# Kernel tuning notes

Measured on AMD Instinct MI355X. Metric: run time of the kernel, lower is better.

Reference implementation:

```python
import jax, jax.numpy as jnp
import numpy as np

B, S, D = 2, 2048, 2048
H, KV, HD = 32, 8, 64
REP = H // KV  # query heads per kv head
SCALE = np.float32(1.0 / np.sqrt(HD))


def setup_inputs() -> dict:
    key = jax.random.key(0)
    ks = jax.random.split(key, 5)
    x = jax.random.normal(ks[0], (B, S, D), dtype=jnp.float32)
    # RoPE tables: standard rotate_half convention, cos/sin shape [S, HD]
    inv_freq = 1.0 / (10000.0 ** (jnp.arange(0, HD, 2, dtype=jnp.float32) / HD))
    freqs = jnp.outer(jnp.arange(S, dtype=jnp.float32), inv_freq)  # [S, HD/2]
    emb = jnp.concatenate([freqs, freqs], axis=-1)  # [S, HD]
    cos, sin = jnp.cos(emb), jnp.sin(emb)
    std = np.float32(0.02)
    Wq = jax.random.normal(ks[1], (D, H * HD), dtype=jnp.float32) * std
    Wk = jax.random.normal(ks[2], (D, KV * HD), dtype=jnp.float32) * std
    Wv = jax.random.normal(ks[3], (D, KV * HD), dtype=jnp.float32) * std
    Wo = jax.random.normal(ks[4], (H * HD, D), dtype=jnp.float32) * std
    return {"x": x, "cos": cos, "sin": sin, "Wq": Wq, "Wk": Wk, "Wv": Wv, "Wo": Wo}


def _rotate_half(u):
    u1, u2 = jnp.split(u, 2, axis=-1)
    return jnp.concatenate([-u2, u1], axis=-1)


def reference(x, cos, sin, Wq, Wk, Wv, Wo):
    # projections -> [B, heads, S, HD]
    q = (x @ Wq).reshape(B, S, H, HD).transpose(0, 2, 1, 3)
    k = (x @ Wk).reshape(B, S, KV, HD).transpose(0, 2, 1, 3)
    v = (x @ Wv).reshape(B, S, KV, HD).transpose(0, 2, 1, 3)
    # RoPE on q and k (cos/sin broadcast over batch & head dims)
    c, s = cos[None, None], sin[None, None]
    q = q * c + _rotate_half(q) * s
    k = k * c + _rotate_half(k) * s
    # GQA: group query heads per kv head instead of materializing repeat_kv
    qg = q.reshape(B, KV, REP, S, HD)
    scores = jnp.einsum('bgrqd,bgkd->bgrqk', qg, k) * SCALE  # [B,KV,REP,S,S]
    causal = jnp.tril(jnp.ones((S, S), dtype=bool))
    scores = jnp.where(causal, scores, jnp.float32(-1e30))
    attn = jax.nn.softmax(scores, axis=-1)
    out = jnp.einsum('bgrqk,bgkd->bgrqd', attn, v)  # [B,KV,REP,S,HD]
    out = out.reshape(B, H, S, HD).transpose(0, 2, 1, 3).reshape(B, S, H * HD)
    return out @ Wo
```

## Files before the change

### kernel.cpp

```cpp
#include <hip/hip_runtime.h>

typedef unsigned short u16;
typedef __bf16 bfx8 __attribute__((ext_vector_type(8)));
typedef float f32x4 __attribute__((ext_vector_type(4)));
typedef float f32x16 __attribute__((ext_vector_type(16)));

#define MFMA16(a,b,c) __builtin_amdgcn_mfma_f32_16x16x32_bf16(a,b,c,0,0,0)
#define MFMA32(a,b,c) __builtin_amdgcn_mfma_f32_32x32x16_bf16(a,b,c,0,0,0)

__device__ __forceinline__ u16 f2bf(float f) {
  union { float f; unsigned u; } v; v.f = f;
  unsigned r = v.u + 0x7fffu + ((v.u >> 16) & 1u);
  return (u16)(r >> 16);
}

__device__ __forceinline__ unsigned cvtpk(float lo, float hi) {
  unsigned r;
  asm("v_cvt_pk_bf16_f32 %0, %1, %2" : "=v"(r) : "v"(lo), "v"(hi));
  return r;
}

__device__ __forceinline__ void swap32(unsigned &a, unsigned &b) {
  asm("v_permlane32_swap_b32 %0, %1" : "+v"(a), "+v"(b));
}

__device__ __forceinline__ void gld16(const void* g, void* l) {
  __builtin_amdgcn_global_load_lds(
      (const __attribute__((address_space(1))) unsigned int*)g,
      (__attribute__((address_space(3))) unsigned int*)l, 16, 0, 0);
}


__global__ void afrag_k(const float* __restrict__ in, u16* __restrict__ Af) {
  int i = blockIdx.x * 256 + threadIdx.x;
  int sm = i >> 8, d0 = (i & 255) * 8;
  const float* p = in + (size_t)sm * 2048 + d0;
  float4 a = *(const float4*)p;
  float4 b = *(const float4*)(p + 4);
  union { u16 h[8]; uint4 u; } o;
  o.h[0]=f2bf(a.x); o.h[1]=f2bf(a.y); o.h[2]=f2bf(a.z); o.h[3]=f2bf(a.w);
  o.h[4]=f2bf(b.x); o.h[5]=f2bf(b.y); o.h[6]=f2bf(b.z); o.h[7]=f2bf(b.w);
  int mt = sm >> 4, kt = d0 >> 5, lp = (sm & 15) + ((d0 >> 3) & 3) * 16;
  *(uint4*)(Af + ((size_t)(mt * 64 + kt) * 512 + lp * 8)) = o.u;
}

__global__ void bfrag_k(const float* __restrict__ W, u16* __restrict__ Bf,
                        int N, int ntoff) {
  __shared__ float tile[32][72];
  int nb = blockIdx.x, kb = blockIdx.y;
  int t = threadIdx.x;
  int r = t >> 3, c8 = (t & 7) * 8;
  const float* src = W + (size_t)(kb * 32 + r) * N + nb * 64 + c8;
  *(float4*)&tile[r][c8]     = *(const float4*)src;
  *(float4*)&tile[r][c8 + 4] = *(const float4*)(src + 4);
  __syncthreads();
  int fb = t >> 6, l = t & 63;
  int nn = fb * 16 + (l & 15), k0 = (l >> 4) * 8;
  union { u16 h[8]; uint4 u; } o;
  #pragma unroll
  for (int j = 0; j < 8; j++) o.h[j] = f2bf(tile[k0 + j][nn]);
  *(uint4*)(Bf + ((size_t)((ntoff + nb * 4 + fb) * 64 + kb) * 512 + l * 8)) = o.u;
}

__global__ __launch_bounds__(256, 3) void gemm_qkv(
    const u16* __restrict__ Af, const u16* __restrict__ Bf,
    const float* __restrict__ cosT, const float* __restrict__ sinT,
    u16* __restrict__ Qf, u16* __restrict__ Kf, u16* __restrict__ Vf) {
  __shared__ u16 lds[2 * 20 * 512];
  const int tid = threadIdx.x, lane = tid & 63, w = tid >> 6;
  const int lrow = lane & 15, lg = lane >> 4;
  const int nwg = gridDim.x;
  const int per = nwg >> 3;
  const int swz = ((int)blockIdx.x & 7) * per + ((int)blockIdx.x >> 3);
  const int bm = swz / 12, bn = swz % 12;
  const int bm4 = bm * 4, bn16 = bn * 16;
  const int KT = 64;

  f32x4 acc[4][4] = {};
  u16* buf0 = lds;
  u16* buf1 = lds + 20 * 512;

  auto stageB = [&](int s, u16* dst) {
    #pragma unroll
    for (int j = 0; j < 4; j++) {
      int ng = w * 4 + j;
      gld16(Bf + ((size_t)(bn16 + ng) * KT + s) * 512 + lane * 8,
            dst + (4 + ng) * 512);
    }
  };
  auto stageA = [&](int s, u16* dst) {
    gld16(Af + ((size_t)(bm4 + w) * KT + s) * 512 + lane * 8,
          dst + w * 512);
  };

  stageB(0, buf0); stageA(0, buf0);
  stageB(1, buf1); stageA(1, buf1);
  asm volatile("s_waitcnt vmcnt(5)" ::: "memory");
  __builtin_amdgcn_s_barrier();

  bfx8 ar[2], br[4];
  for (int t = 0; t < KT; t++) {
    u16* rb = (t & 1) ? buf1 : buf0;
    const int s2 = (t + 2 < KT) ? t + 2 : 0;
    #pragma unroll
    for (int i = 0; i < 2; i++)
      ar[i] = *(const bfx8*)(rb + i * 512 + lane * 8);
    #pragma unroll
    for (int j = 0; j < 4; j++)
      br[j] = *(const bfx8*)(rb + (4 + w * 4 + j) * 512 + lane * 8);
    asm volatile("s_waitcnt lgkmcnt(0)" ::: "memory");
    __builtin_amdgcn_s_barrier();
    stageB(s2, rb);
    __builtin_amdgcn_s_setprio(1);
    #pragma unroll
    for (int i = 0; i < 2; i++)
      #pragma unroll
      for (int j = 0; j < 4; j++)
        acc[i][j] = MFMA16(ar[i], br[j], acc[i][j]);
    __builtin_amdgcn_s_setprio(0);
    __builtin_amdgcn_s_barrier();
    #pragma unroll
    for (int i = 0; i < 2; i++)
      ar[i] = *(const bfx8*)(rb + (2 + i) * 512 + lane * 8);
    asm volatile("s_waitcnt lgkmcnt(0)" ::: "memory");
    __builtin_amdgcn_s_barrier();
    stageA(s2, rb);
    __builtin_amdgcn_s_setprio(1);
    #pragma unroll
    for (int i = 0; i < 2; i++)
      #pragma unroll
      for (int j = 0; j < 4; j++)
        acc[2 + i][j] = MFMA16(ar[i], br[j], acc[2 + i][j]);
    __builtin_amdgcn_s_setprio(0);
    asm volatile("s_waitcnt vmcnt(5)" ::: "memory");
    __builtin_amdgcn_s_barrier();
  }
  asm volatile("s_waitcnt vmcnt(0)" ::: "memory");
  __builtin_amdgcn_s_barrier();

  const int hh = bn * 4 + w;
  const int m0 = bm * 64;
  u16* otw = lds + w * 2048;
  char* otb = (char*)otw;

  #pragma unroll
  for (int half = 0; half < 2; half++) {
    const int rowbase = m0 + half * 32;
    const int bb = rowbase >> 11;
    const int s0 = rowbase & 2047;
    if (hh < 40) {
      const float qsc = (hh < 32) ? 0.18033688f : 1.0f;
      #pragma unroll
      for (int mgl = 0; mgl < 2; mgl++) {
        const int mg = half * 2 + mgl;
        #pragma unroll
        for (int ng = 0; ng < 2; ng++) {
          const int d1 = ng * 16 + lrow;
          #pragma unroll
          for (int r = 0; r < 4; r++) {
            int s = s0 + mgl * 16 + lg * 4 + r;
            float a  = acc[mg][ng][r];
            float a2 = acc[mg][ng + 2][r];
            float c1 = cosT[s * 64 + d1],      s1v = sinT[s * 64 + d1];
            float c2 = cosT[s * 64 + d1 + 32], s2v = sinT[s * 64 + d1 + 32];
            float o1 = (a * c1 - a2 * s1v) * qsc;
            float o2 = (a2 * c2 + a * s2v) * qsc;
            int srow = mgl * 16 + lg * 4 + r;
            int swzb = (srow & 7) << 4;
            *(u16*)(otb + ((srow * 128 + d1 * 2) ^ swzb)) = f2bf(o1);
            *(u16*)(otb + ((srow * 128 + (d1 + 32) * 2) ^ swzb)) = f2bf(o2);
          }
        }
      }
      const int qt = s0 >> 5;
      u16* dst = (hh < 32)
          ? Qf + ((size_t)(bb * 32 + hh) * 64 + qt) * 2048
          : Kf + ((size_t)(bb * 8 + (hh - 32)) * 64 + qt) * 2048;
      const int srw = lane & 31;
      const int d0 = (lane >> 5) * 8;
      #pragma unroll
      for (int ks = 0; ks < 4; ks++) {
        int byte = ((srw * 128 + (ks * 16 + d0) * 2)) ^ ((srw & 7) << 4);
        uint4 v = *(uint4*)(otb + byte);
        *(uint4*)(dst + ks * 512 + lane * 8) = v;
      }
    } else {
      #pragma unroll
      for (int mgl = 0; mgl < 2; mgl++) {
        const int mg = half * 2 + mgl;
        #pragma unroll
        for (int ng = 0; ng < 4; ng++) {
          const int d = ng * 16 + lrow;
          #pragma unroll
          for (int r = 0; r < 4; r++) {
            int srow = mgl * 16 + lg * 4 + r;
            *(u16*)(otb + ((srow * 128 + d * 2) ^ ((srow & 7) << 4))) =
                f2bf(acc[mg][ng][r]);
          }
        }
      }
      const int kt = s0 >> 6;
      const int g = hh - 40;
      u16* dst = Vf + ((size_t)(bb * 8 + g) * 32 + kt) * 4096;
      const int d = lane & 31;
      const int hi8 = (lane >> 5) * 8;
      #pragma unroll
      for (int ks2 = 0; ks2 < 2; ks2++) {
        const int ks = half * 2 + ks2;
        #pragma unroll
        for (int sub = 0; sub < 2; sub++) {
          const int dd = sub * 32 + d;
          union { u16 h[8]; uint4 u; } o;
          #pragma unroll
          for (int j = 0; j < 8; j++) {
            int srow = ks2 * 16 + hi8 + j;
            o.h[j] = *(u16*)(otb + ((srow * 128 + dd * 2) ^ ((srow & 7) << 4)));
          }
          *(uint4*)(dst + (sub * 4 + ks) * 512 + lane * 8) = o.u;
        }
      }
    }
    __builtin_amdgcn_s_barrier();
  }
}

__global__ __launch_bounds__(256, 3) void gemm8p(
    const u16* __restrict__ Af, const u16* __restrict__ Bf,
    float* __restrict__ C, int N, int KT, int nbx) {
  __shared__ u16 lds[2 * 20 * 512];
  const int tid = threadIdx.x, lane = tid & 63, w = tid >> 6;
  const int lrow = lane & 15, lg = lane >> 4;
  const int nwg = gridDim.x;
  const int per = nwg >> 3;
  const int swz = ((int)blockIdx.x & 7) * per + ((int)blockIdx.x >> 3);
  const int bm = swz / nbx, bn = swz % nbx;
  const int bm4 = bm * 4, bn16 = bn * 16;
  const int T = KT;

  f32x4 acc[4][4] = {};
  u16* buf0 = lds;
  u16* buf1 = lds + 20 * 512;

  auto stageB = [&](int s, u16* dst) {
    #pragma unroll
    for (int j = 0; j < 4; j++) {
      int ng = w * 4 + j;
      gld16(Bf + ((size_t)(bn16 + ng) * KT + s) * 512 + lane * 8,
            dst + (4 + ng) * 512);
    }
  };
  auto stageA = [&](int s, u16* dst) {
    gld16(Af + ((size_t)(bm4 + w) * KT + s) * 512 + lane * 8,
          dst + w * 512);
  };

  stageB(0, buf0); stageA(0, buf0);
  stageB(1, buf1); stageA(1, buf1);
  asm volatile("s_waitcnt vmcnt(5)" ::: "memory");
  __builtin_amdgcn_s_barrier();

  bfx8 ar[2], br[4];
  for (int t = 0; t < T; t++) {
    u16* rb = (t & 1) ? buf1 : buf0;
    const int s2 = (t + 2 < T) ? t + 2 : 0;
    #pragma unroll
    for (int i = 0; i < 2; i++)
      ar[i] = *(const bfx8*)(rb + i * 512 + lane * 8);
    #pragma unroll
    for (int j = 0; j < 4; j++)
      br[j] = *(const bfx8*)(rb + (4 + w * 4 + j) * 512 + lane * 8);
    asm volatile("s_waitcnt lgkmcnt(0)" ::: "memory");
    __builtin_amdgcn_s_barrier();
    stageB(s2, rb);
    __builtin_amdgcn_s_setprio(1);
    #pragma unroll
    for (int i = 0; i < 2; i++)
      #pragma unroll
      for (int j = 0; j < 4; j++)
        acc[i][j] = MFMA16(ar[i], br[j], acc[i][j]);
    __builtin_amdgcn_s_setprio(0);
    __builtin_amdgcn_s_barrier();
    #pragma unroll
    for (int i = 0; i < 2; i++)
      ar[i] = *(const bfx8*)(rb + (2 + i) * 512 + lane * 8);
    asm volatile("s_waitcnt lgkmcnt(0)" ::: "memory");
    __builtin_amdgcn_s_barrier();
    stageA(s2, rb);
    __builtin_amdgcn_s_setprio(1);
    #pragma unroll
    for (int i = 0; i < 2; i++)
      #pragma unroll
      for (int j = 0; j < 4; j++)
        acc[2 + i][j] = MFMA16(ar[i], br[j], acc[2 + i][j]);
    __builtin_amdgcn_s_setprio(0);
    asm volatile("s_waitcnt vmcnt(5)" ::: "memory");
    __builtin_amdgcn_s_barrier();
  }
  asm volatile("s_waitcnt vmcnt(0)" ::: "memory");

  const int m0 = bm * 64, n0 = bn * 256 + w * 64;
  #pragma unroll
  for (int mg = 0; mg < 4; mg++) {
    int row = m0 + mg * 16 + lg * 4;
    #pragma unroll
    for (int ng = 0; ng < 4; ng++) {
      int col = n0 + ng * 16 + lrow;
      float* cp = C + (size_t)row * N + col;
      #pragma unroll
      for (int r = 0; r < 4; r++) cp[(size_t)r * N] = acc[mg][ng][r];
    }
  }
}

__global__ __launch_bounds__(256, 2) void attn_k(
    const u16* __restrict__ Qf, const u16* __restrict__ Kf,
    const u16* __restrict__ Vf, u16* __restrict__ Aof)
{
  __shared__ u16 ot[4][32 * 64];
  const int tid = threadIdx.x, lane = tid & 63, w = tid >> 6;
  const int h = blockIdx.y, b = blockIdx.z;
  const int kvh = h >> 2;
  const int ql = lane & 31, hi = lane >> 5;
  const int qrA = blockIdx.x * 4 + w;

  const u16* Qh = Qf + (size_t)(b * 32 + h) * 131072;
  const u16* Kp = Kf + (size_t)(b * 8 + kvh) * 131072 + lane * 8;
  const u16* Vp = Vf + (size_t)(b * 8 + kvh) * 131072 + lane * 8;

  #pragma unroll
  for (int half = 0; half < 2; half++) {
    const int qr = half ? qrA : 63 - qrA;
    const int q0 = qr * 32;
    const int qg = q0 + ql;
    const int nkt = qr / 2 + 1;

    bfx8 qf[4];
    #pragma unroll
    for (int ks = 0; ks < 4; ks++)
      qf[ks] = *(const bfx8*)(Qh + (size_t)qr * 2048 + ks * 512 + lane * 8);

    f32x16 oacc0 = {}, oacc1 = {};
    float lsv[8] = {};

    const u16* Kt = Kp;
    const u16* Vt = Vp;
    bfx8 ka[8];
    #pragma unroll
    for (int i = 0; i < 8; i++)
      ka[i] = *(const bfx8*)(Kt + i * 512);

    #pragma unroll 2
    for (int kt = 0; kt < nkt; kt++) {
      const int kb = kt * 64;
      bfx8 va[8];
      #pragma unroll
      for (int i = 0; i < 8; i++)
        va[i] = *(const bfx8*)(Vt + i * 512);
      f32x16 st0 = {}, st1 = {};
      #pragma unroll
      for (int ks = 0; ks < 4; ks++) {
        st0 = MFMA32(ka[ks], qf[ks], st0);
        st1 = MFMA32(ka[4 + ks], qf[ks], st1);
      }
      const u16* Kn = (kt + 1 < nkt) ? Kt + 4096 : Kp;
      bfx8 kn[8];
      #pragma unroll
      for (int i = 0; i < 8; i++)
        kn[i] = *(const bfx8*)(Kn + i * 512);
      if (kt == nkt - 1) {
        #pragma unroll
        for (int r = 0; r < 16; r++) {
          int crow = (r & 3) + 8 * (r >> 2) + 4 * hi;
          if (kb + crow > qg) st0[r] = -3.0e38f;
          if (kb + 32 + crow > qg) st1[r] = -3.0e38f;
        }
      }
      #pragma unroll
      for (int r = 0; r < 16; r++) { st0[r] = exp2f(st0[r]); }
      #pragma unroll
      for (int r = 0; r < 16; r++) { st1[r] = exp2f(st1[r]); }
      #pragma unroll
      for (int r = 0; r < 16; r++) lsv[r & 7] += st0[r] + st1[r];
      bfx8 pb[4];
      #pragma unroll
      for (int ks = 0; ks < 4; ks++) {
        int o = (ks & 1) * 8;
        unsigned X = cvtpk(ks < 2 ? st0[o + 0] : st1[o + 0], ks < 2 ? st0[o + 1] : st1[o + 1]);
        unsigned Z = cvtpk(ks < 2 ? st0[o + 2] : st1[o + 2], ks < 2 ? st0[o + 3] : st1[o + 3]);
        unsigned Y = cvtpk(ks < 2 ? st0[o + 4] : st1[o + 4], ks < 2 ? st0[o + 5] : st1[o + 5]);
        unsigned W = cvtpk(ks < 2 ? st0[o + 6] : st1[o + 6], ks < 2 ? st0[o + 7] : st1[o + 7]);
        swap32(X, Y);
        swap32(Z, W);
        union { unsigned u[4]; bfx8 v; } uu;
        uu.u[0] = X; uu.u[1] = Z; uu.u[2] = Y; uu.u[3] = W;
        pb[ks] = uu.v;
      }
      #pragma unroll
      for (int ks = 0; ks < 4; ks++) {
        oacc0 = MFMA32(va[ks], pb[ks], oacc0);
        oacc1 = MFMA32(va[4 + ks], pb[ks], oacc1);
      }
      #pragma unroll
      for (int i = 0; i < 8; i++) ka[i] = kn[i];
      Kt += 4096;
      Vt += 4096;
    }
    float lsum = ((lsv[0] + lsv[1]) + (lsv[2] + lsv[3])) +
                 ((lsv[4] + lsv[5]) + (lsv[6] + lsv[7]));
    lsum += __shfl_xor(lsum, 32);
    float inv = 1.f / lsum;
    u16* my = ot[w];
    #pragma unroll
    for (int dt = 0; dt < 2; dt++) {
      #pragma unroll
      for (int g = 0; g < 4; g++) {
        float a0 = (dt ? oacc1[g*4+0] : oacc0[g*4+0]) * inv;
        float a1 = (dt ? oacc1[g*4+1] : oacc0[g*4+1]) * inv;
        float a2 = (dt ? oacc1[g*4+2] : oacc0[g*4+2]) * inv;
        float a3 = (dt ? oacc1[g*4+3] : oacc0[g*4+3]) * inv;
        unsigned w0 = cvtpk(a0, a1), w1 = cvtpk(a2, a3);
        int d = dt * 32 + g * 8 + 4 * hi;
        int byte = (ql * 128 + d * 2) ^ ((ql & 7) << 4);
        *(uint2*)((char*)my + byte) = make_uint2(w0, w1);
      }
    }
    #pragma unroll
    for (int rr = 0; rr < 4; rr++) {
      int q = rr * 8 + (lane >> 3);
      int dk = (lane & 7) * 8;
      int byte = (q * 128 + dk * 2) ^ ((q & 7) << 4);
      uint4 val = *(uint4*)((char*)my + byte);
      int mt = b * 128 + qr * 2 + (q >> 4);
      int ktg = h * 2 + (dk >> 5);
      int lp = (q & 15) + ((dk >> 3) & 3) * 16;
      *(uint4*)(Aof + ((size_t)(mt * 64 + ktg) * 512 + lp * 8)) = val;
    }
  }
}

extern "C" void kernel_launch(void* const* d_in, const int* in_sizes, int n_in,
                              void* d_out, int out_size, void* d_ws, size_t ws_size,
                              hipStream_t stream) {
  const float* x    = (const float*)d_in[0];
  const float* cosT = (const float*)d_in[1];
  const float* sinT = (const float*)d_in[2];
  const float* Wq   = (const float*)d_in[3];
  const float* Wk   = (const float*)d_in[4];
  const float* Wv   = (const float*)d_in[5];
  const float* Wo   = (const float*)d_in[6];
  float* out = (float*)d_out;
  char* ws = (char*)d_ws;

  u16* Af   = (u16*)(ws);
  u16* Bqkv = (u16*)(ws + 16777216);
  u16* Bwo  = (u16*)(ws + 29360128);
  u16* Qf   = (u16*)(ws + 37748736);
  u16* Kf   = (u16*)(ws + 54525952);
  u16* Vf   = (u16*)(ws + 58720256);
  u16* Aof  = (u16*)(ws + 62914560);

  afrag_k<<<4096, 256, 0, stream>>>(x, Af);
  bfrag_k<<<dim3(32, 64), 256, 0, stream>>>(Wq, Bqkv, 2048, 0);
  bfrag_k<<<dim3(8, 64), 256, 0, stream>>>(Wk, Bqkv, 512, 128);
  bfrag_k<<<dim3(8, 64), 256, 0, stream>>>(Wv, Bqkv, 512, 160);
  bfrag_k<<<dim3(32, 64), 256, 0, stream>>>(Wo, Bwo, 2048, 0);

  gemm_qkv<<<768, 256, 0, stream>>>(Af, Bqkv, cosT, sinT, Qf, Kf, Vf);

  attn_k<<<dim3(8, 32, 2), 256, 0, stream>>>(Qf, Kf, Vf, Aof);

  gemm8p<<<512, 256, 0, stream>>>(Aof, Bwo, out, 2048, 64, 8);
}
```

Measured before the change: 186.8 us.

## Enlarge QKV GEMM tile to 256x256 with 8 waves and 4-stage LDS ring

The fused QKV projection GEMM moves from 256-thread blocks with 64-row M tiles to 512-thread blocks that each cover 256 rows, with 8 waves laid out 2x4. Global loads go into a four-slot LDS ring prefetched three K-steps ahead instead of double buffering. The aim is more operand reuse per LDS load, less global traffic and deeper latency hiding. In exchange there is more LDS (128KB) and more accumulator registers, and only 192 workgroups, which may leave CUs poorly occupied. The epilogue is adapted to write four 32-row chunks per wave, and the per-chunk barrier is dropped.

```diff
diff --git a/kernel.cpp b/kernel.cpp
--- a/kernel.cpp
+++ b/kernel.cpp
@@ -62,97 +62,97 @@
   *(uint4*)(Bf + ((size_t)((ntoff + nb * 4 + fb) * 64 + kb) * 512 + l * 8)) = o.u;
 }
 
-__global__ __launch_bounds__(256, 3) void gemm_qkv(
+__global__ __launch_bounds__(512, 2) void gemm_qkv(
     const u16* __restrict__ Af, const u16* __restrict__ Bf,
     const float* __restrict__ cosT, const float* __restrict__ sinT,
     u16* __restrict__ Qf, u16* __restrict__ Kf, u16* __restrict__ Vf) {
-  __shared__ u16 lds[2 * 20 * 512];
+  __shared__ u16 lds[65536];
   const int tid = threadIdx.x, lane = tid & 63, w = tid >> 6;
+  const int wm = w >> 2, wn = w & 3;
   const int lrow = lane & 15, lg = lane >> 4;
   const int nwg = gridDim.x;
   const int per = nwg >> 3;
   const int swz = ((int)blockIdx.x & 7) * per + ((int)blockIdx.x >> 3);
   const int bm = swz / 12, bn = swz % 12;
-  const int bm4 = bm * 4, bn16 = bn * 16;
-  const int KT = 64;
-
-  f32x4 acc[4][4] = {};
-  u16* buf0 = lds;
-  u16* buf1 = lds + 20 * 512;
-
-  auto stageB = [&](int s, u16* dst) {
-    #pragma unroll
-    for (int j = 0; j < 4; j++) {
-      int ng = w * 4 + j;
-      gld16(Bf + ((size_t)(bn16 + ng) * KT + s) * 512 + lane * 8,
-            dst + (4 + ng) * 512);
+  const int bm16 = bm * 16, bn16 = bn * 16;
+  const int NG = 64;
+
+  f32x4 acc[8][4] = {};
+
+  auto stage2 = [&](int g, int ph) {
+    int gs = (g < NG) ? g : 0;
+    u16* sl = lds + (g & 3) * 16384;
+    #pragma unroll
+    for (int j = 0; j < 2; j++) {
+      int bi = w * 4 + ph * 2 + j;
+      const u16* src = (bi < 16)
+        ? Af + ((size_t)(bm16 + bi) * NG + gs) * 512 + lane * 8
+        : Bf + ((size_t)(bn16 + (bi - 16)) * NG + gs) * 512 + lane * 8;
+      gld16(src, sl + bi * 512);
     }
   };
-  auto stageA = [&](int s, u16* dst) {
-    gld16(Af + ((size_t)(bm4 + w) * KT + s) * 512 + lane * 8,
-          dst + w * 512);
-  };
-
-  stageB(0, buf0); stageA(0, buf0);
-  stageB(1, buf1); stageA(1, buf1);
-  asm volatile("s_waitcnt vmcnt(5)" ::: "memory");
+
+  stage2(0, 0); stage2(0, 1);
+  stage2(1, 0); stage2(1, 1);
+  stage2(2, 0); stage2(2, 1);
+  asm volatile("s_waitcnt vmcnt(8)" ::: "memory");
   __builtin_amdgcn_s_barrier();
 
-  bfx8 ar[2], br[4];
-  for (int t = 0; t < KT; t++) {
-    u16* rb = (t & 1) ? buf1 : buf0;
-    const int s2 = (t + 2 < KT) ? t + 2 : 0;
-    #pragma unroll
-    for (int i = 0; i < 2; i++)
-      ar[i] = *(const bfx8*)(rb + i * 512 + lane * 8);
+  bfx8 ar[4], br[4];
+  for (int g = 0; g < NG; g++) {
+    u16* sl = lds + (g & 3) * 16384;
     #pragma unroll
     for (int j = 0; j < 4; j++)
-      br[j] = *(const bfx8*)(rb + (4 + w * 4 + j) * 512 + lane * 8);
+      br[j] = *(const bfx8*)(sl + (16 + wn * 4 + j) * 512 + lane * 8);
+    #pragma unroll
+    for (int i = 0; i < 4; i++)
+      ar[i] = *(const bfx8*)(sl + (wm * 8 + i) * 512 + lane * 8);
+    stage2(g + 3, 0);
+    __builtin_amdgcn_s_barrier();
     asm volatile("s_waitcnt lgkmcnt(0)" ::: "memory");
-    __builtin_amdgcn_s_barrier();
-    stageB(s2, rb);
+    __builtin_amdgcn_sched_barrier(0);
     __builtin_amdgcn_s_setprio(1);
     #pragma unroll
-    for (int i = 0; i < 2; i++)
+    for (int i = 0; i < 4; i++)
       #pragma unroll
       for (int j = 0; j < 4; j++)
         acc[i][j] = MFMA16(ar[i], br[j], acc[i][j]);
     __builtin_amdgcn_s_setprio(0);
     __builtin_amdgcn_s_barrier();
     #pragma unroll
-    for (int i = 0; i < 2; i++)
-      ar[i] = *(const bfx8*)(rb + (2 + i) * 512 + lane * 8);
+    for (int i = 0; i < 4; i++)
+      ar[i] = *(const bfx8*)(sl + (wm * 8 + 4 + i) * 512 + lane * 8);
+    stage2(g + 3, 1);
+    __builtin_amdgcn_s_barrier();
     asm volatile("s_waitcnt lgkmcnt(0)" ::: "memory");
-    __builtin_amdgcn_s_barrier();
-    stageA(s2, rb);
+    __builtin_amdgcn_sched_barrier(0);
     __builtin_amdgcn_s_setprio(1);
     #pragma unroll
-    for (int i = 0; i < 2; i++)
+    for (int i = 0; i < 4; i++)
       #pragma unroll
       for (int j = 0; j < 4; j++)
-        acc[2 + i][j] = MFMA16(ar[i], br[j], acc[2 + i][j]);
+        acc[4 + i][j] = MFMA16(ar[i], br[j], acc[4 + i][j]);
     __builtin_amdgcn_s_setprio(0);
-    asm volatile("s_waitcnt vmcnt(5)" ::: "memory");
+    asm volatile("s_waitcnt vmcnt(8)" ::: "memory");
     __builtin_amdgcn_s_barrier();
   }
   asm volatile("s_waitcnt vmcnt(0)" ::: "memory");
   __builtin_amdgcn_s_barrier();
 
-  const int hh = bn * 4 + w;
-  const int m0 = bm * 64;
-  u16* otw = lds + w * 2048;
-  char* otb = (char*)otw;
+  const int hh = bn * 4 + wn;
+  const int m0 = bm * 256 + wm * 128;
+  char* otb = (char*)(lds + w * 2048);
 
   #pragma unroll
-  for (int half = 0; half < 2; half++) {
-    const int rowbase = m0 + half * 32;
+  for (int c = 0; c < 4; c++) {
+    const int rowbase = m0 + c * 32;
     const int bb = rowbase >> 11;
     const int s0 = rowbase & 2047;
     if (hh < 40) {
       const float qsc = (hh < 32) ? 0.18033688f : 1.0f;
       #pragma unroll
       for (int mgl = 0; mgl < 2; mgl++) {
-        const int mg = half * 2 + mgl;
+        const int mg = c * 2 + mgl;
         #pragma unroll
         for (int ng = 0; ng < 2; ng++) {
           const int d1 = ng * 16 + lrow;
@@ -187,7 +187,7 @@
     } else {
       #pragma unroll
       for (int mgl = 0; mgl < 2; mgl++) {
-        const int mg = half * 2 + mgl;
+        const int mg = c * 2 + mgl;
         #pragma unroll
         for (int ng = 0; ng < 4; ng++) {
           const int d = ng * 16 + lrow;
@@ -200,13 +200,14 @@
         }
       }
       const int kt = s0 >> 6;
+      const int vh = (s0 >> 5) & 1;
       const int g = hh - 40;
       u16* dst = Vf + ((size_t)(bb * 8 + g) * 32 + kt) * 4096;
       const int d = lane & 31;
       const int hi8 = (lane >> 5) * 8;
       #pragma unroll
       for (int ks2 = 0; ks2 < 2; ks2++) {
-        const int ks = half * 2 + ks2;
+        const int ks = vh * 2 + ks2;
         #pragma unroll
         for (int sub = 0; sub < 2; sub++) {
           const int dd = sub * 32 + d;
@@ -220,7 +221,6 @@
         }
       }
     }
-    __builtin_amdgcn_s_barrier();
   }
 }
 
@@ -465,7 +465,7 @@
   bfrag_k<<<dim3(8, 64), 256, 0, stream>>>(Wv, Bqkv, 512, 160);
   bfrag_k<<<dim3(32, 64), 256, 0, stream>>>(Wo, Bwo, 2048, 0);
 
-  gemm_qkv<<<768, 256, 0, stream>>>(Af, Bqkv, cosT, sinT, Qf, Kf, Vf);
+  gemm_qkv<<<192, 512, 0, stream>>>(Af, Bqkv, cosT, sinT, Qf, Kf, Vf);
 
   attn_k<<<dim3(8, 32, 2), 256, 0, stream>>>(Qf, Kf, Vf, Aof);
 
```

Result: no change. 186.0 us, median of 2 (-0.5%).

## Software-pipeline QK^T one tile ahead of softmax and PV in attention loop

Applied to the files above, without the earlier changes.

Restructures the key-tile loop so the QK^T MFMAs for tile kt+1 run while tile kt's exp2, bf16 packing and PV MFMAs execute, and K loads are prefetched two tiles ahead. The aim is to let matrix-core work overlap with the transcendental and VALU work and to hide global-load latency. In exchange it holds an extra pair of f32x16 score accumulators and a second K register buffer, which raises VGPR pressure and may lower occupancy or cause spills. On the final iteration it computes a redundant QK^T on a dummy tile.

```diff
diff --git a/kernel.cpp b/kernel.cpp
--- a/kernel.cpp
+++ b/kernel.cpp
@@ -344,10 +344,24 @@
 
     const u16* Kt = Kp;
     const u16* Vt = Vp;
-    bfx8 ka[8];
+
+    f32x16 sA0 = {}, sA1 = {};
+    {
+      bfx8 k0[8];
+      #pragma unroll
+      for (int i = 0; i < 8; i++)
+        k0[i] = *(const bfx8*)(Kt + i * 512);
+      #pragma unroll
+      for (int ks = 0; ks < 4; ks++) {
+        sA0 = MFMA32(k0[ks], qf[ks], sA0);
+        sA1 = MFMA32(k0[4 + ks], qf[ks], sA1);
+      }
+    }
+    const u16* Kn1 = (nkt > 1) ? Kt + 4096 : Kp;
+    bfx8 kn[8];
     #pragma unroll
     for (int i = 0; i < 8; i++)
-      ka[i] = *(const bfx8*)(Kt + i * 512);
+      kn[i] = *(const bfx8*)(Kn1 + i * 512);
 
     #pragma unroll 2
     for (int kt = 0; kt < nkt; kt++) {
@@ -356,39 +370,39 @@
       #pragma unroll
       for (int i = 0; i < 8; i++)
         va[i] = *(const bfx8*)(Vt + i * 512);
-      f32x16 st0 = {}, st1 = {};
+      const u16* Kn2 = (kt + 2 < nkt) ? Kt + 2 * 4096 : Kp;
+      bfx8 knn[8];
+      #pragma unroll
+      for (int i = 0; i < 8; i++)
+        knn[i] = *(const bfx8*)(Kn2 + i * 512);
+      f32x16 sB0 = {}, sB1 = {};
       #pragma unroll
       for (int ks = 0; ks < 4; ks++) {
-        st0 = MFMA32(ka[ks], qf[ks], st0);
-        st1 = MFMA32(ka[4 + ks], qf[ks], st1);
-      }
-      const u16* Kn = (kt + 1 < nkt) ? Kt + 4096 : Kp;
-      bfx8 kn[8];
-      #pragma unroll
-      for (int i = 0; i < 8; i++)
-        kn[i] = *(const bfx8*)(Kn + i * 512);
+        sB0 = MFMA32(kn[ks], qf[ks], sB0);
+        sB1 = MFMA32(kn[4 + ks], qf[ks], sB1);
+      }
       if (kt == nkt - 1) {
         #pragma unroll
         for (int r = 0; r < 16; r++) {
           int crow = (r & 3) + 8 * (r >> 2) + 4 * hi;
-          if (kb + crow > qg) st0[r] = -3.0e38f;
-          if (kb + 32 + crow > qg) st1[r] = -3.0e38f;
+          if (kb + crow > qg) sA0[r] = -3.0e38f;
+          if (kb + 32 + crow > qg) sA1[r] = -3.0e38f;
         }
       }
       #pragma unroll
-      for (int r = 0; r < 16; r++) { st0[r] = exp2f(st0[r]); }
-      #pragma unroll
-      for (int r = 0; r < 16; r++) { st1[r] = exp2f(st1[r]); }
-      #pragma unroll
-      for (int r = 0; r < 16; r++) lsv[r & 7] += st0[r] + st1[r];
+      for (int r = 0; r < 16; r++) { sA0[r] = exp2f(sA0[r]); }
+      #pragma unroll
+      for (int r = 0; r < 16; r++) { sA1[r] = exp2f(sA1[r]); }
+      #pragma unroll
+      for (int r = 0; r < 16; r++) lsv[r & 7] += sA0[r] + sA1[r];
       bfx8 pb[4];
       #pragma unroll
       for (int ks = 0; ks < 4; ks++) {
         int o = (ks & 1) * 8;
-        unsigned X = cvtpk(ks < 2 ? st0[o + 0] : st1[o + 0], ks < 2 ? st0[o + 1] : st1[o + 1]);
-        unsigned Z = cvtpk(ks < 2 ? st0[o + 2] : st1[o + 2], ks < 2 ? st0[o + 3] : st1[o + 3]);
-        unsigned Y = cvtpk(ks < 2 ? st0[o + 4] : st1[o + 4], ks < 2 ? st0[o + 5] : st1[o + 5]);
-        unsigned W = cvtpk(ks < 2 ? st0[o + 6] : st1[o + 6], ks < 2 ? st0[o + 7] : st1[o + 7]);
+        unsigned X = cvtpk(ks < 2 ? sA0[o + 0] : sA1[o + 0], ks < 2 ? sA0[o + 1] : sA1[o + 1]);
+        unsigned Z = cvtpk(ks < 2 ? sA0[o + 2] : sA1[o + 2], ks < 2 ? sA0[o + 3] : sA1[o + 3]);
+        unsigned Y = cvtpk(ks < 2 ? sA0[o + 4] : sA1[o + 4], ks < 2 ? sA0[o + 5] : sA1[o + 5]);
+        unsigned W = cvtpk(ks < 2 ? sA0[o + 6] : sA1[o + 6], ks < 2 ? sA0[o + 7] : sA1[o + 7]);
         swap32(X, Y);
         swap32(Z, W);
         union { unsigned u[4]; bfx8 v; } uu;
@@ -401,7 +415,9 @@
         oacc1 = MFMA32(va[4 + ks], pb[ks], oacc1);
       }
       #pragma unroll
-      for (int i = 0; i < 8; i++) ka[i] = kn[i];
+      for (int i = 0; i < 8; i++) kn[i] = knn[i];
+      sA0 = sB0;
+      sA1 = sB1;
       Kt += 4096;
       Vt += 4096;
     }
```

After: 190.5 us. About the same (+2.0%).
